# Kernel optimization log

Measured on AMD Instinct MI355X. Metric: run time of the kernel, lower is better.

Reference implementation:

```python
import jax, jax.numpy as jnp
import numpy as np

N_ATOMS = 50000
N_PAIRS = 1000000
F = 128        # n_atombasis
K = 64         # n_radialbasis
B = 5          # graph_n_blocks
NRI = 3        # residual layers (interaction)
NRF = 2        # residual layers (features)
_LOG2 = float(np.log(2.0))


def ssp(x):
    # shifted softplus: log(0.5*exp(x) + 0.5)
    return jax.nn.softplus(x) - _LOG2


def setup_inputs() -> dict:
    key = jax.random.key(0)
    ks = jax.random.split(key, 24)
    s = 0.1
    f32 = jnp.float32
    inp = {
        'features': jax.random.normal(ks[0], (N_ATOMS, F), f32),
        'cutoffs': jax.random.uniform(ks[1], (N_PAIRS,), f32),
        'rbfs': jax.random.uniform(ks[2], (N_PAIRS, K), f32),
        'idx_i': jnp.sort(jax.random.randint(ks[3], (N_PAIRS,), 0, N_ATOMS)),
        'idx_j': jax.random.randint(ks[4], (N_PAIRS,), 0, N_ATOMS),
        # per-block parameters (leading dim = block)
        'Wg': jax.random.normal(ks[5], (B, K, F), f32) * s,      # rbf filter, no bias
        'Wi': jax.random.normal(ks[6], (B, F, F), f32) * s,
        'bi': jnp.zeros((B, F), f32),
        'Wj': jax.random.normal(ks[7], (B, F, F), f32) * s,
        'bj': jnp.zeros((B, F), f32),
        'Wr1': jax.random.normal(ks[8], (B, NRI, F, F), f32) * s,
        'br1': jnp.zeros((B, NRI, F), f32),
        'Wr2': jax.random.normal(ks[9], (B, NRI, F, F), f32) * s,
        'br2': jnp.zeros((B, NRI, F), f32),
        'Wout': jax.random.normal(ks[10], (B, F, F), f32) * s,
        'bout': jnp.zeros((B, F), f32),
        'u': jnp.ones((B, F), f32),                               # gated skip
        'Wf1': jax.random.normal(ks[11], (B, NRF, F, F), f32) * s,
        'bf1': jnp.zeros((B, NRF, F), f32),
        'Wf2': jax.random.normal(ks[12], (B, NRF, F, F), f32) * s,
        'bf2': jnp.zeros((B, NRF, F), f32),
    }
    return inp


def _physnet_forward(features, cutoffs, rbfs, idx_i, idx_j,
                     Wg, Wi, bi, Wj, bj, Wr1, br1, Wr2, br2,
                     Wout, bout, u, Wf1, bf1, Wf2, bf2):
    descriptors = cutoffs[:, None] * rbfs           # [P, K]
    x = features
    outs = []
    for b in range(B):
        xa = ssp(x)
        g = descriptors @ Wg[b]                     # [P, F]
        xi = ssp(xa @ Wi[b] + bi[b])                # [N, F]
        xj = ssp(xa @ Wj[b] + bj[b])                # [N, F]
        msg = g * xj[idx_j]                         # gather-transform, [P, F]
        m = xi + jax.ops.segment_sum(msg, idx_i, num_segments=N_ATOMS)
        for r in range(NRI):                        # residual (interaction)
            m = m + ssp(ssp(m) @ Wr1[b, r] + br1[b, r]) @ Wr2[b, r] + br2[b, r]
        m = ssp(m)
        x = u[b] * x + m @ Wout[b] + bout[b]        # gated update
        for r in range(NRF):                        # residual (features)
            x = x + ssp(ssp(x) @ Wf1[b, r] + bf1[b, r]) @ Wf2[b, r] + bf2[b, r]
        outs.append(x)
    return jnp.stack(outs, axis=0)                  # [B, N, F] == features_list


def reference(features, cutoffs, rbfs, idx_i, idx_j,
              Wg, Wi, bi, Wj, bj, Wr1, br1, Wr2, br2,
              Wout, bout, u, Wf1, bf1, Wf2, bf2):
    return _physnet_forward(features, cutoffs, rbfs, idx_i, idx_j,
                            Wg, Wi, bi, Wj, bj, Wr1, br1, Wr2, br2,
                            Wout, bout, u, Wf1, bf1, Wf2, bf2)
```

## Files before the change

kernel.cpp:

```cpp
#include <hip/hip_runtime.h>
#include <math.h>

#define NA 50000
#define NP 1000000
#define FD 128
#define KD 64
#define NB 5
#define NRI_ 3
#define NRF_ 2

typedef short short8_t __attribute__((ext_vector_type(8)));
typedef short short4_t __attribute__((ext_vector_type(4)));
typedef float f32x4 __attribute__((ext_vector_type(4)));

__device__ __forceinline__ float sspf(float x) {
    float t = __logf(__expf(-fabsf(x)) + 1.0f);
    return fmaxf(x, 0.0f) + (t - 0.69314718055994530942f);
}

__device__ __forceinline__ unsigned cvt_pk_bf16(float lo, float hi) {
    unsigned r;
    asm("v_cvt_pk_bf16_f32 %0, %1, %2" : "=v"(r) : "v"(lo), "v"(hi));
    return r;
}

__device__ __forceinline__ short f2bf(float f) {
    unsigned r;
    asm("v_cvt_pk_bf16_f32 %0, %1, %1" : "=v"(r) : "v"(f));
    return (short)r;
}

__global__ void transpose_weights(const float* __restrict__ src,
                                  short* __restrict__ dst, int K)
{
    const size_t mo = (size_t)blockIdx.x * K * 128;
    const float* s = src + mo;
    short* d = dst + mo;
    for (int e = threadIdx.x; e < K * 128; e += 256) {
        int k = e >> 7, n = e & 127;
        d[n * K + k] = f2bf(s[e]);
    }
}

__global__ void prep_desc(const float* __restrict__ rbfs,
                          const float* __restrict__ cutoffs,
                          short* __restrict__ desc)
{
    long long c = (long long)blockIdx.x * 256 + threadIdx.x;
    if (c >= (long long)NP * 8) return;
    long long pair = c >> 3;
    float cu = cutoffs[pair];
    const float* s = rbfs + c * 8;
    float4 a = *(const float4*)s;
    float4 b = *(const float4*)(s + 4);
    int4 pk;
    pk.x = (int)cvt_pk_bf16(a.x * cu, a.y * cu);
    pk.y = (int)cvt_pk_bf16(a.z * cu, a.w * cu);
    pk.z = (int)cvt_pk_bf16(b.x * cu, b.y * cu);
    pk.w = (int)cvt_pk_bf16(b.z * cu, b.w * cu);
    *(int4*)&desc[c * 8] = pk;
}

__device__ __forceinline__ void stage_wt(const short* __restrict__ WT,
                                         short* wt_s, int tid)
{
#pragma unroll
    for (int i = 0; i < 8; ++i) {
        int c = i * 256 + tid;
        int n = c >> 4, kc = c & 15;
        *(short8_t*)&wt_s[n * 136 + kc * 8] = *(const short8_t*)&WT[n * 128 + kc * 8];
    }
}

__device__ __forceinline__ void gemm16(const short* actw, const short* wt_s,
                                       int mI, int quad, f32x4 acc[8])
{
#pragma unroll
    for (int ch = 0; ch < 4; ++ch) {
        short8_t a = *(const short8_t*)&actw[mI * 136 + ch * 32 + quad * 8];
#pragma unroll
        for (int ct = 0; ct < 8; ++ct) {
            short8_t bf = *(const short8_t*)&wt_s[(ct * 16 + mI) * 136 + ch * 32 + quad * 8];
            acc[ct] = __builtin_amdgcn_mfma_f32_16x16x32_bf16(a, bf, acc[ct], 0, 0, 0);
        }
    }
}

__launch_bounds__(256, 3)
__global__ void pre_kernel(const float* __restrict__ x,
                           const short* __restrict__ WiT, const float* __restrict__ bi_,
                           const short* __restrict__ WjT, const float* __restrict__ bj_,
                           float* __restrict__ xi_out, float* __restrict__ xj_out)
{
    __shared__ short act_s[64 * 136];
    __shared__ short wt_s[128 * 136];
    const int tid = threadIdx.x;
    const int lane = tid & 63, wv = tid >> 6;
    const int mI = lane & 15, quad = lane >> 4;
    const short* actw = act_s + wv * 16 * 136;
    const int row0 = blockIdx.x * 64;
    const int rowrd = row0 + wv * 16 + quad * 4;

#pragma unroll
    for (int i = 0; i < 8; ++i) {
        int f = i * 256 + tid;
        int rr = f >> 5;
        int c4 = (f & 31) * 4;
        float4 v = make_float4(0.f, 0.f, 0.f, 0.f);
        if (row0 + rr < NA) v = *(const float4*)&x[(size_t)(row0 + rr) * FD + c4];
        int2 pk;
        pk.x = (int)cvt_pk_bf16(sspf(v.x), sspf(v.y));
        pk.y = (int)cvt_pk_bf16(sspf(v.z), sspf(v.w));
        *(int2*)&act_s[rr * 136 + c4] = pk;
    }
    stage_wt(WiT, wt_s, tid);
    __syncthreads();

    f32x4 acc[8];
#pragma unroll
    for (int ct = 0; ct < 8; ++ct) acc[ct] = (f32x4){0.f, 0.f, 0.f, 0.f};
    gemm16(actw, wt_s, mI, quad, acc);
#pragma unroll
    for (int ct = 0; ct < 8; ++ct) {
        float bb = bi_[ct * 16 + mI];
#pragma unroll
        for (int rg = 0; rg < 4; ++rg) {
            int r = rowrd + rg;
            if (r < NA) xi_out[(size_t)r * FD + ct * 16 + mI] = sspf(acc[ct][rg] + bb);
        }
    }
    __syncthreads();
    stage_wt(WjT, wt_s, tid);
    __syncthreads();
#pragma unroll
    for (int ct = 0; ct < 8; ++ct) acc[ct] = (f32x4){0.f, 0.f, 0.f, 0.f};
    gemm16(actw, wt_s, mI, quad, acc);
#pragma unroll
    for (int ct = 0; ct < 8; ++ct) {
        float bb = bj_[ct * 16 + mI];
#pragma unroll
        for (int rg = 0; rg < 4; ++rg) {
            int r = rowrd + rg;
            if (r < NA) xj_out[(size_t)r * FD + ct * 16 + mI] = sspf(acc[ct][rg] + bb);
        }
    }
}

template<bool TAIL>
__launch_bounds__(256, 3)
__global__ void chain_kernel(const float* __restrict__ xprev,
                             const float* __restrict__ mbuf,
                             const short* __restrict__ Wr1T, const float* __restrict__ br1_,
                             const short* __restrict__ Wr2T, const float* __restrict__ br2_,
                             const short* __restrict__ WoT,  const float* __restrict__ bo_,
                             const float* __restrict__ u_,
                             const short* __restrict__ Wf1T, const float* __restrict__ bf1_,
                             const short* __restrict__ Wf2T, const float* __restrict__ bf2_,
                             float* __restrict__ xout,
                             const short* __restrict__ WiT, const float* __restrict__ bi_,
                             const short* __restrict__ WjT, const float* __restrict__ bj_,
                             float* __restrict__ xi_out, float* __restrict__ xj_out)
{
    __shared__ short act_s[64 * 136];
    __shared__ short wt_s[128 * 136];
    const int tid = threadIdx.x;
    const int lane = tid & 63, wv = tid >> 6;
    const int mI = lane & 15, quad = lane >> 4;
    short* actw = act_s + wv * 16 * 136;
    const int rowrd = blockIdx.x * 64 + wv * 16 + quad * 4;

    float mreg[8][4];
#pragma unroll
    for (int ct = 0; ct < 8; ++ct)
#pragma unroll
        for (int rg = 0; rg < 4; ++rg) {
            int r = rowrd + rg;
            mreg[ct][rg] = (r < NA) ? mbuf[(size_t)r * FD + ct * 16 + mI] : 0.f;
        }

    f32x4 acc[8];

    for (int r = 0; r < NRI_; ++r) {
        __syncthreads();
        stage_wt(Wr1T + (size_t)r * FD * FD, wt_s, tid);
#pragma unroll
        for (int ct = 0; ct < 8; ++ct)
#pragma unroll
            for (int rg = 0; rg < 4; ++rg)
                actw[(quad * 4 + rg) * 136 + ct * 16 + mI] = f2bf(sspf(mreg[ct][rg]));
        __syncthreads();
#pragma unroll
        for (int ct = 0; ct < 8; ++ct) acc[ct] = (f32x4){0.f, 0.f, 0.f, 0.f};
        gemm16(actw, wt_s, mI, quad, acc);

        __syncthreads();
        stage_wt(Wr2T + (size_t)r * FD * FD, wt_s, tid);
#pragma unroll
        for (int ct = 0; ct < 8; ++ct) {
            float b1 = br1_[r * FD + ct * 16 + mI];
#pragma unroll
            for (int rg = 0; rg < 4; ++rg)
                actw[(quad * 4 + rg) * 136 + ct * 16 + mI] = f2bf(sspf(acc[ct][rg] + b1));
        }
        __syncthreads();
#pragma unroll
        for (int ct = 0; ct < 8; ++ct) acc[ct] = (f32x4){0.f, 0.f, 0.f, 0.f};
        gemm16(actw, wt_s, mI, quad, acc);
#pragma unroll
        for (int ct = 0; ct < 8; ++ct) {
            float b2 = br2_[r * FD + ct * 16 + mI];
#pragma unroll
            for (int rg = 0; rg < 4; ++rg)
                mreg[ct][rg] += acc[ct][rg] + b2;
        }
    }

    __syncthreads();
    stage_wt(WoT, wt_s, tid);
#pragma unroll
    for (int ct = 0; ct < 8; ++ct)
#pragma unroll
        for (int rg = 0; rg < 4; ++rg)
            actw[(quad * 4 + rg) * 136 + ct * 16 + mI] = f2bf(sspf(mreg[ct][rg]));
    __syncthreads();
#pragma unroll
    for (int ct = 0; ct < 8; ++ct) acc[ct] = (f32x4){0.f, 0.f, 0.f, 0.f};
    gemm16(actw, wt_s, mI, quad, acc);

    float xreg[8][4];
#pragma unroll
    for (int ct = 0; ct < 8; ++ct) {
        float bo = bo_[ct * 16 + mI];
        float uu = u_[ct * 16 + mI];
#pragma unroll
        for (int rg = 0; rg < 4; ++rg) {
            int r = rowrd + rg;
            float xp = (r < NA) ? xprev[(size_t)r * FD + ct * 16 + mI] : 0.f;
            xreg[ct][rg] = fmaf(uu, xp, acc[ct][rg] + bo);
        }
    }

    for (int r = 0; r < NRF_; ++r) {
        __syncthreads();
        stage_wt(Wf1T + (size_t)r * FD * FD, wt_s, tid);
#pragma unroll
        for (int ct = 0; ct < 8; ++ct)
#pragma unroll
            for (int rg = 0; rg < 4; ++rg)
                actw[(quad * 4 + rg) * 136 + ct * 16 + mI] = f2bf(sspf(xreg[ct][rg]));
        __syncthreads();
#pragma unroll
        for (int ct = 0; ct < 8; ++ct) acc[ct] = (f32x4){0.f, 0.f, 0.f, 0.f};
        gemm16(actw, wt_s, mI, quad, acc);

        __syncthreads();
        stage_wt(Wf2T + (size_t)r * FD * FD, wt_s, tid);
#pragma unroll
        for (int ct = 0; ct < 8; ++ct) {
            float b1 = bf1_[r * FD + ct * 16 + mI];
#pragma unroll
            for (int rg = 0; rg < 4; ++rg)
                actw[(quad * 4 + rg) * 136 + ct * 16 + mI] = f2bf(sspf(acc[ct][rg] + b1));
        }
        __syncthreads();
#pragma unroll
        for (int ct = 0; ct < 8; ++ct) acc[ct] = (f32x4){0.f, 0.f, 0.f, 0.f};
        gemm16(actw, wt_s, mI, quad, acc);
#pragma unroll
        for (int ct = 0; ct < 8; ++ct) {
            float b2 = bf2_[r * FD + ct * 16 + mI];
#pragma unroll
            for (int rg = 0; rg < 4; ++rg)
                xreg[ct][rg] += acc[ct][rg] + b2;
        }
    }

#pragma unroll
    for (int ct = 0; ct < 8; ++ct)
#pragma unroll
        for (int rg = 0; rg < 4; ++rg) {
            int r = rowrd + rg;
            if (r < NA) xout[(size_t)r * FD + ct * 16 + mI] = xreg[ct][rg];
        }

    if constexpr (TAIL) {
        __syncthreads();
        stage_wt(WiT, wt_s, tid);
#pragma unroll
        for (int ct = 0; ct < 8; ++ct)
#pragma unroll
            for (int rg = 0; rg < 4; ++rg)
                actw[(quad * 4 + rg) * 136 + ct * 16 + mI] = f2bf(sspf(xreg[ct][rg]));
        __syncthreads();
#pragma unroll
        for (int ct = 0; ct < 8; ++ct) acc[ct] = (f32x4){0.f, 0.f, 0.f, 0.f};
        gemm16(actw, wt_s, mI, quad, acc);
#pragma unroll
        for (int ct = 0; ct < 8; ++ct) {
            float bb = bi_[ct * 16 + mI];
#pragma unroll
            for (int rg = 0; rg < 4; ++rg) {
                int r = rowrd + rg;
                if (r < NA) xi_out[(size_t)r * FD + ct * 16 + mI] = sspf(acc[ct][rg] + bb);
            }
        }
        __syncthreads();
        stage_wt(WjT, wt_s, tid);
        __syncthreads();
#pragma unroll
        for (int ct = 0; ct < 8; ++ct) acc[ct] = (f32x4){0.f, 0.f, 0.f, 0.f};
        gemm16(actw, wt_s, mI, quad, acc);
#pragma unroll
        for (int ct = 0; ct < 8; ++ct) {
            float bb = bj_[ct * 16 + mI];
#pragma unroll
            for (int rg = 0; rg < 4; ++rg) {
                int r = rowrd + rg;
                if (r < NA) xj_out[(size_t)r * FD + ct * 16 + mI] = sspf(acc[ct][rg] + bb);
            }
        }
    }
}

template<bool DESC>
__launch_bounds__(256, 4)
__global__ void pair_mfma(const float* __restrict__ rbfs,
                          const float* __restrict__ cutoffs,
                          const short* __restrict__ desc,
                          const int* __restrict__ idx_i,
                          const int* __restrict__ idx_j,
                          const short* __restrict__ WgT,
                          const float* __restrict__ xj,
                          float* __restrict__ mout)
{
    __shared__ float g_s[64 * 132];
    __shared__ int ii_s[128];
    __shared__ int jj_s[128];
    short* wt_s = (short*)g_s;

    const int tid = threadIdx.x;
    const long long p0 = (long long)blockIdx.x * 128;

#pragma unroll
    for (int i = 0; i < 4; ++i) {
        int c = i * 256 + tid;
        int n = c >> 3, kc = c & 7;
        *(short8_t*)&wt_s[n * 72 + kc * 8] = *(const short8_t*)&WgT[n * 64 + kc * 8];
    }
    if (tid < 128) {
        long long pg = p0 + tid;
        ii_s[tid] = (pg < NP) ? idx_i[pg] : -1;
        jj_s[tid] = (pg < NP) ? idx_j[pg] : 0;
    }
    __syncthreads();

    const int lane = tid & 63, wv = tid >> 6;
    const int m = lane & 15, quad = lane >> 4;

    f32x4 acc[2][8];
#pragma unroll
    for (int rt = 0; rt < 2; ++rt)
#pragma unroll
        for (int ct = 0; ct < 8; ++ct) acc[rt][ct] = (f32x4){0.f, 0.f, 0.f, 0.f};

#pragma unroll
    for (int chunk = 0; chunk < 2; ++chunk) {
        short8_t afr[2];
#pragma unroll
        for (int rt = 0; rt < 2; ++rt) {
            long long pg = p0 + wv * 32 + rt * 16 + m;
            if constexpr (DESC) {
                if (pg < NP) {
                    afr[rt] = *(const short8_t*)&desc[pg * KD + chunk * 32 + quad * 8];
                } else {
                    int4 z = make_int4(0, 0, 0, 0);
                    afr[rt] = __builtin_bit_cast(short8_t, z);
                }
            } else {
                float v[8];
                if (pg < NP) {
                    const float* ap = rbfs + pg * KD + chunk * 32 + quad * 8;
                    float4 x0 = *(const float4*)ap;
                    float4 x1 = *(const float4*)(ap + 4);
                    float cu = cutoffs[pg];
                    v[0] = x0.x * cu; v[1] = x0.y * cu; v[2] = x0.z * cu; v[3] = x0.w * cu;
                    v[4] = x1.x * cu; v[5] = x1.y * cu; v[6] = x1.z * cu; v[7] = x1.w * cu;
                } else {
#pragma unroll
                    for (int j = 0; j < 8; ++j) v[j] = 0.f;
                }
                int4 pk = make_int4((int)cvt_pk_bf16(v[0], v[1]),
                                    (int)cvt_pk_bf16(v[2], v[3]),
                                    (int)cvt_pk_bf16(v[4], v[5]),
                                    (int)cvt_pk_bf16(v[6], v[7]));
                afr[rt] = __builtin_bit_cast(short8_t, pk);
            }
        }
#pragma unroll
        for (int ct = 0; ct < 8; ++ct) {
            short8_t bfr = *(short8_t*)&wt_s[(ct * 16 + m) * 72 + chunk * 32 + quad * 8];
            acc[0][ct] = __builtin_amdgcn_mfma_f32_16x16x32_bf16(afr[0], bfr, acc[0][ct], 0, 0, 0);
            acc[1][ct] = __builtin_amdgcn_mfma_f32_16x16x32_bf16(afr[1], bfr, acc[1][ct], 0, 0, 0);
        }
    }
    __syncthreads();

    const int tx = tid & 15, ty = tid >> 4;
    const int c0 = tx * 4, c1 = c0 + 64;
    const int col = tid & 127, sh = tid >> 7;

#pragma unroll
    for (int h = 0; h < 2; ++h) {
        if ((wv >> 1) == h) {
#pragma unroll
            for (int ct = 0; ct < 8; ++ct) {
                int cg = ct * 16 + m;
#pragma unroll
                for (int rt = 0; rt < 2; ++rt) {
                    int lp = (wv & 1) * 32 + rt * 16 + quad * 4;
#pragma unroll
                    for (int rg = 0; rg < 4; ++rg)
                        g_s[(lp + rg) * 132 + cg] = acc[rt][ct][rg];
                }
            }
        }
        __syncthreads();
#pragma unroll
        for (int i = 0; i < 4; ++i) {
            int p = ty + 16 * i;
            int jrow = jj_s[h * 64 + p];
            float4 xa = *(const float4*)&xj[(size_t)jrow * FD + c0];
            float4 xb = *(const float4*)&xj[(size_t)jrow * FD + c1];
            float4 ga = *(float4*)&g_s[p * 132 + c0];
            float4 gb = *(float4*)&g_s[p * 132 + c1];
            ga.x *= xa.x; ga.y *= xa.y; ga.z *= xa.z; ga.w *= xa.w;
            gb.x *= xb.x; gb.y *= xb.y; gb.z *= xb.z; gb.w *= xb.w;
            *(float4*)&g_s[p * 132 + c0] = ga;
            *(float4*)&g_s[p * 132 + c1] = gb;
        }
        __syncthreads();
        {
            int base = h * 64 + sh * 32;
            float accum = 0.f;
            int cur = ii_s[base];
            for (int q = 0; q < 32; ++q) {
                int a = ii_s[base + q];
                if (a != cur) {
                    if (cur >= 0) atomicAdd(&mout[(size_t)cur * FD + col], accum);
                    accum = 0.f;
                    cur = a;
                }
                accum += g_s[(sh * 32 + q) * 132 + col];
            }
            if (cur >= 0) atomicAdd(&mout[(size_t)cur * FD + col], accum);
        }
        if (h == 0) __syncthreads();
    }
}

extern "C" void kernel_launch(void* const* d_in, const int* in_sizes, int n_in,
                              void* d_out, int out_size, void* d_ws, size_t ws_size,
                              hipStream_t stream)
{
    const float* features = (const float*)d_in[0];
    const float* cutoffs  = (const float*)d_in[1];
    const float* rbfs     = (const float*)d_in[2];
    const int*   idx_i    = (const int*)d_in[3];
    const int*   idx_j    = (const int*)d_in[4];
    const float* Wg   = (const float*)d_in[5];
    const float* Wi   = (const float*)d_in[6];
    const float* bi   = (const float*)d_in[7];
    const float* Wj   = (const float*)d_in[8];
    const float* bj   = (const float*)d_in[9];
    const float* Wr1  = (const float*)d_in[10];
    const float* br1  = (const float*)d_in[11];
    const float* Wr2  = (const float*)d_in[12];
    const float* br2  = (const float*)d_in[13];
    const float* Wout = (const float*)d_in[14];
    const float* bout = (const float*)d_in[15];
    const float* u    = (const float*)d_in[16];
    const float* Wf1  = (const float*)d_in[17];
    const float* bf1  = (const float*)d_in[18];
    const float* Wf2  = (const float*)d_in[19];
    const float* bf2  = (const float*)d_in[20];
    float* out = (float*)d_out;

    const size_t NF = (size_t)NA * FD;
    const size_t MS = (size_t)FD * FD;
    float* mbuf = (float*)d_ws;
    short* wtb  = (short*)(mbuf + NF);
    short* wgt  = wtb + 65 * MS;
    short* desc = wgt + (size_t)NB * FD * KD;
    float* xjbuf = out + 4 * NF;

    const size_t base_bytes = NF * 4 + 65 * MS * 2 + (size_t)NB * FD * KD * 2;
    const size_t desc_bytes = (size_t)NP * KD * 2;
    const bool use_desc = ws_size >= base_bytes + desc_bytes;

    transpose_weights<<<5,  256, 0, stream>>>(Wi,   wtb +  0 * MS, 128);
    transpose_weights<<<5,  256, 0, stream>>>(Wj,   wtb +  5 * MS, 128);
    transpose_weights<<<15, 256, 0, stream>>>(Wr1,  wtb + 10 * MS, 128);
    transpose_weights<<<15, 256, 0, stream>>>(Wr2,  wtb + 25 * MS, 128);
    transpose_weights<<<5,  256, 0, stream>>>(Wout, wtb + 40 * MS, 128);
    transpose_weights<<<10, 256, 0, stream>>>(Wf1,  wtb + 45 * MS, 128);
    transpose_weights<<<10, 256, 0, stream>>>(Wf2,  wtb + 55 * MS, 128);
    transpose_weights<<<5,  256, 0, stream>>>(Wg,   wgt, 64);
    if (use_desc) {
        prep_desc<<<(int)(((long long)NP * 8 + 255) / 256), 256, 0, stream>>>(rbfs, cutoffs, desc);
    }

    const int gA = (NA + 63) / 64;
    const int gP = (NP + 127) / 128;
    dim3 blk(256);

    pre_kernel<<<gA, blk, 0, stream>>>(features,
        wtb + 0 * MS, bi, wtb + 5 * MS, bj, mbuf, xjbuf);

    const float* x = features;
    for (int b = 0; b < NB; ++b) {
        float* xout = out + (size_t)b * NF;

        if (use_desc) {
            pair_mfma<true><<<gP, blk, 0, stream>>>(rbfs, cutoffs, desc, idx_i, idx_j,
                wgt + (size_t)b * FD * KD, xjbuf, mbuf);
        } else {
            pair_mfma<false><<<gP, blk, 0, stream>>>(rbfs, cutoffs, desc, idx_i, idx_j,
                wgt + (size_t)b * FD * KD, xjbuf, mbuf);
        }

        if (b < NB - 1) {
            chain_kernel<true><<<gA, blk, 0, stream>>>(x, mbuf,
                wtb + (10 + b * NRI_) * MS, br1 + (size_t)b * NRI_ * FD,
                wtb + (25 + b * NRI_) * MS, br2 + (size_t)b * NRI_ * FD,
                wtb + (40 + b) * MS, bout + (size_t)b * FD, u + (size_t)b * FD,
                wtb + (45 + b * NRF_) * MS, bf1 + (size_t)b * NRF_ * FD,
                wtb + (55 + b * NRF_) * MS, bf2 + (size_t)b * NRF_ * FD,
                xout,
                wtb + (0 + (b + 1)) * MS, bi + (size_t)(b + 1) * FD,
                wtb + (5 + (b + 1)) * MS, bj + (size_t)(b + 1) * FD,
                mbuf, xjbuf);
        } else {
            chain_kernel<false><<<gA, blk, 0, stream>>>(x, mbuf,
                wtb + (10 + b * NRI_) * MS, br1 + (size_t)b * NRI_ * FD,
                wtb + (25 + b * NRI_) * MS, br2 + (size_t)b * NRI_ * FD,
                wtb + (40 + b) * MS, bout + (size_t)b * FD, u + (size_t)b * FD,
                wtb + (45 + b * NRF_) * MS, bf1 + (size_t)b * NRF_ * FD,
                wtb + (55 + b * NRF_) * MS, bf2 + (size_t)b * NRF_ * FD,
                xout,
                (const short*)nullptr, (const float*)nullptr,
                (const short*)nullptr, (const float*)nullptr,
                (float*)nullptr, (float*)nullptr);
        }
        x = xout;
    }
}
```

Before: 2.113 ms.

## Pre-swizzle weights and descriptors into MFMA fragment order, read from global

Weights and the rbf descriptor buffer are now pre-packed into the exact per-lane MFMA B/A fragment order, so each lane loads one contiguous 16-byte vector straight from global or L2. The kernels drop LDS weight staging along with most of their __syncthreads, and occupancy hints rise from 3 to 4 blocks because LDS use shrinks. The trade-off is that weight fragments are re-read from cache by every wave instead of being shared through LDS, which adds L2 traffic and load latency to the MFMA loops. Removing the barriers also depends on each wave touching only its own slice of act_s.

```diff
diff --git a/kernel.cpp b/kernel.cpp
--- a/kernel.cpp
+++ b/kernel.cpp
@@ -10,7 +10,6 @@
 #define NRF_ 2
 
 typedef short short8_t __attribute__((ext_vector_type(8)));
-typedef short short4_t __attribute__((ext_vector_type(4)));
 typedef float f32x4 __attribute__((ext_vector_type(4)));
 
 __device__ __forceinline__ float sspf(float x) {
@@ -30,27 +29,40 @@
     return (short)r;
 }
 
-__global__ void transpose_weights(const float* __restrict__ src,
-                                  short* __restrict__ dst, int K)
-{
-    const size_t mo = (size_t)blockIdx.x * K * 128;
-    const float* s = src + mo;
-    short* d = dst + mo;
-    for (int e = threadIdx.x; e < K * 128; e += 256) {
-        int k = e >> 7, n = e & 127;
-        d[n * K + k] = f2bf(s[e]);
+__global__ void frag_weights(const float* __restrict__ src,
+                             short* __restrict__ dst, int kch)
+{
+    const int nchunk = kch * 512;
+    const float* s = src + (size_t)blockIdx.x * kch * 4096;
+    short* d = dst + (size_t)blockIdx.x * kch * 4096;
+    for (int c = threadIdx.x; c < nchunk; c += 256) {
+        int lane = c & 63, ct = (c >> 6) & 7, ch = c >> 9;
+        int quad = lane >> 4, mI = lane & 15;
+        const float* sp = s + (ch * 32 + quad * 8) * 128 + ct * 16 + mI;
+        float v[8];
+#pragma unroll
+        for (int j = 0; j < 8; ++j) v[j] = sp[j * 128];
+        int4 pk = make_int4((int)cvt_pk_bf16(v[0], v[1]),
+                            (int)cvt_pk_bf16(v[2], v[3]),
+                            (int)cvt_pk_bf16(v[4], v[5]),
+                            (int)cvt_pk_bf16(v[6], v[7]));
+        *(short8_t*)&d[c * 8] = __builtin_bit_cast(short8_t, pk);
     }
 }
 
 __global__ void prep_desc(const float* __restrict__ rbfs,
                           const float* __restrict__ cutoffs,
-                          short* __restrict__ desc)
+                          short* __restrict__ descF)
 {
     long long c = (long long)blockIdx.x * 256 + threadIdx.x;
     if (c >= (long long)NP * 8) return;
-    long long pair = c >> 3;
-    float cu = cutoffs[pair];
-    const float* s = rbfs + c * 8;
+    int lane = (int)(c & 63);
+    int chunk = (int)((c >> 6) & 1);
+    long long t16 = c >> 7;
+    int quad = lane >> 4, mI = lane & 15;
+    long long p = t16 * 16 + mI;
+    float cu = cutoffs[p];
+    const float* s = rbfs + p * KD + chunk * 32 + quad * 8;
     float4 a = *(const float4*)s;
     float4 b = *(const float4*)(s + 4);
     int4 pk;
@@ -58,42 +70,32 @@
     pk.y = (int)cvt_pk_bf16(a.z * cu, a.w * cu);
     pk.z = (int)cvt_pk_bf16(b.x * cu, b.y * cu);
     pk.w = (int)cvt_pk_bf16(b.z * cu, b.w * cu);
-    *(int4*)&desc[c * 8] = pk;
-}
-
-__device__ __forceinline__ void stage_wt(const short* __restrict__ WT,
-                                         short* wt_s, int tid)
-{
-#pragma unroll
-    for (int i = 0; i < 8; ++i) {
-        int c = i * 256 + tid;
-        int n = c >> 4, kc = c & 15;
-        *(short8_t*)&wt_s[n * 136 + kc * 8] = *(const short8_t*)&WT[n * 128 + kc * 8];
-    }
-}
-
-__device__ __forceinline__ void gemm16(const short* actw, const short* wt_s,
-                                       int mI, int quad, f32x4 acc[8])
+    *(short8_t*)&descF[c * 8] = __builtin_bit_cast(short8_t, pk);
+}
+
+__device__ __forceinline__ void gemm16_direct(const short* actw,
+                                              const short* __restrict__ WF,
+                                              int mI, int quad, int lane,
+                                              f32x4 acc[8])
 {
 #pragma unroll
     for (int ch = 0; ch < 4; ++ch) {
         short8_t a = *(const short8_t*)&actw[mI * 136 + ch * 32 + quad * 8];
 #pragma unroll
         for (int ct = 0; ct < 8; ++ct) {
-            short8_t bf = *(const short8_t*)&wt_s[(ct * 16 + mI) * 136 + ch * 32 + quad * 8];
+            short8_t bf = *(const short8_t*)&WF[((ch * 8 + ct) * 64 + lane) * 8];
             acc[ct] = __builtin_amdgcn_mfma_f32_16x16x32_bf16(a, bf, acc[ct], 0, 0, 0);
         }
     }
 }
 
-__launch_bounds__(256, 3)
+__launch_bounds__(256, 4)
 __global__ void pre_kernel(const float* __restrict__ x,
-                           const short* __restrict__ WiT, const float* __restrict__ bi_,
-                           const short* __restrict__ WjT, const float* __restrict__ bj_,
+                           const short* __restrict__ WiF, const float* __restrict__ bi_,
+                           const short* __restrict__ WjF, const float* __restrict__ bj_,
                            float* __restrict__ xi_out, float* __restrict__ xj_out)
 {
     __shared__ short act_s[64 * 136];
-    __shared__ short wt_s[128 * 136];
     const int tid = threadIdx.x;
     const int lane = tid & 63, wv = tid >> 6;
     const int mI = lane & 15, quad = lane >> 4;
@@ -113,13 +115,12 @@
         pk.y = (int)cvt_pk_bf16(sspf(v.z), sspf(v.w));
         *(int2*)&act_s[rr * 136 + c4] = pk;
     }
-    stage_wt(WiT, wt_s, tid);
     __syncthreads();
 
     f32x4 acc[8];
 #pragma unroll
     for (int ct = 0; ct < 8; ++ct) acc[ct] = (f32x4){0.f, 0.f, 0.f, 0.f};
-    gemm16(actw, wt_s, mI, quad, acc);
+    gemm16_direct(actw, WiF, mI, quad, lane, acc);
 #pragma unroll
     for (int ct = 0; ct < 8; ++ct) {
         float bb = bi_[ct * 16 + mI];
@@ -129,12 +130,9 @@
             if (r < NA) xi_out[(size_t)r * FD + ct * 16 + mI] = sspf(acc[ct][rg] + bb);
         }
     }
-    __syncthreads();
-    stage_wt(WjT, wt_s, tid);
-    __syncthreads();
 #pragma unroll
     for (int ct = 0; ct < 8; ++ct) acc[ct] = (f32x4){0.f, 0.f, 0.f, 0.f};
-    gemm16(actw, wt_s, mI, quad, acc);
+    gemm16_direct(actw, WjF, mI, quad, lane, acc);
 #pragma unroll
     for (int ct = 0; ct < 8; ++ct) {
         float bb = bj_[ct * 16 + mI];
@@ -147,22 +145,21 @@
 }
 
 template<bool TAIL>
-__launch_bounds__(256, 3)
+__launch_bounds__(256, 4)
 __global__ void chain_kernel(const float* __restrict__ xprev,
                              const float* __restrict__ mbuf,
-                             const short* __restrict__ Wr1T, const float* __restrict__ br1_,
-                             const short* __restrict__ Wr2T, const float* __restrict__ br2_,
-                             const short* __restrict__ WoT,  const float* __restrict__ bo_,
+                             const short* __restrict__ Wr1F, const float* __restrict__ br1_,
+                             const short* __restrict__ Wr2F, const float* __restrict__ br2_,
+                             const short* __restrict__ WoF,  const float* __restrict__ bo_,
                              const float* __restrict__ u_,
-                             const short* __restrict__ Wf1T, const float* __restrict__ bf1_,
-                             const short* __restrict__ Wf2T, const float* __restrict__ bf2_,
+                             const short* __restrict__ Wf1F, const float* __restrict__ bf1_,
+                             const short* __restrict__ Wf2F, const float* __restrict__ bf2_,
                              float* __restrict__ xout,
-                             const short* __restrict__ WiT, const float* __restrict__ bi_,
-                             const short* __restrict__ WjT, const float* __restrict__ bj_,
+                             const short* __restrict__ WiF, const float* __restrict__ bi_,
+                             const short* __restrict__ WjF, const float* __restrict__ bj_,
                              float* __restrict__ xi_out, float* __restrict__ xj_out)
 {
     __shared__ short act_s[64 * 136];
-    __shared__ short wt_s[128 * 136];
     const int tid = threadIdx.x;
     const int lane = tid & 63, wv = tid >> 6;
     const int mI = lane & 15, quad = lane >> 4;
@@ -181,20 +178,15 @@
     f32x4 acc[8];
 
     for (int r = 0; r < NRI_; ++r) {
-        __syncthreads();
-        stage_wt(Wr1T + (size_t)r * FD * FD, wt_s, tid);
 #pragma unroll
         for (int ct = 0; ct < 8; ++ct)
 #pragma unroll
             for (int rg = 0; rg < 4; ++rg)
                 actw[(quad * 4 + rg) * 136 + ct * 16 + mI] = f2bf(sspf(mreg[ct][rg]));
-        __syncthreads();
 #pragma unroll
         for (int ct = 0; ct < 8; ++ct) acc[ct] = (f32x4){0.f, 0.f, 0.f, 0.f};
-        gemm16(actw, wt_s, mI, quad, acc);
-
-        __syncthreads();
-        stage_wt(Wr2T + (size_t)r * FD * FD, wt_s, tid);
+        gemm16_direct(actw, Wr1F + (size_t)r * FD * FD, mI, quad, lane, acc);
+
 #pragma unroll
         for (int ct = 0; ct < 8; ++ct) {
             float b1 = br1_[r * FD + ct * 16 + mI];
@@ -202,10 +194,9 @@
             for (int rg = 0; rg < 4; ++rg)
                 actw[(quad * 4 + rg) * 136 + ct * 16 + mI] = f2bf(sspf(acc[ct][rg] + b1));
         }
-        __syncthreads();
 #pragma unroll
         for (int ct = 0; ct < 8; ++ct) acc[ct] = (f32x4){0.f, 0.f, 0.f, 0.f};
-        gemm16(actw, wt_s, mI, quad, acc);
+        gemm16_direct(actw, Wr2F + (size_t)r * FD * FD, mI, quad, lane, acc);
 #pragma unroll
         for (int ct = 0; ct < 8; ++ct) {
             float b2 = br2_[r * FD + ct * 16 + mI];
@@ -215,17 +206,14 @@
         }
     }
 
-    __syncthreads();
-    stage_wt(WoT, wt_s, tid);
 #pragma unroll
     for (int ct = 0; ct < 8; ++ct)
 #pragma unroll
         for (int rg = 0; rg < 4; ++rg)
             actw[(quad * 4 + rg) * 136 + ct * 16 + mI] = f2bf(sspf(mreg[ct][rg]));
-    __syncthreads();
 #pragma unroll
     for (int ct = 0; ct < 8; ++ct) acc[ct] = (f32x4){0.f, 0.f, 0.f, 0.f};
-    gemm16(actw, wt_s, mI, quad, acc);
+    gemm16_direct(actw, WoF, mI, quad, lane, acc);
 
     float xreg[8][4];
 #pragma unroll
@@ -241,20 +229,15 @@
     }
 
     for (int r = 0; r < NRF_; ++r) {
-        __syncthreads();
-        stage_wt(Wf1T + (size_t)r * FD * FD, wt_s, tid);
 #pragma unroll
         for (int ct = 0; ct < 8; ++ct)
 #pragma unroll
             for (int rg = 0; rg < 4; ++rg)
                 actw[(quad * 4 + rg) * 136 + ct * 16 + mI] = f2bf(sspf(xreg[ct][rg]));
-        __syncthreads();
 #pragma unroll
         for (int ct = 0; ct < 8; ++ct) acc[ct] = (f32x4){0.f, 0.f, 0.f, 0.f};
-        gemm16(actw, wt_s, mI, quad, acc);
-
-        __syncthreads();
-        stage_wt(Wf2T + (size_t)r * FD * FD, wt_s, tid);
+        gemm16_direct(actw, Wf1F + (size_t)r * FD * FD, mI, quad, lane, acc);
+
 #pragma unroll
         for (int ct = 0; ct < 8; ++ct) {
             float b1 = bf1_[r * FD + ct * 16 + mI];
@@ -262,10 +245,9 @@
             for (int rg = 0; rg < 4; ++rg)
                 actw[(quad * 4 + rg) * 136 + ct * 16 + mI] = f2bf(sspf(acc[ct][rg] + b1));
         }
-        __syncthreads();
 #pragma unroll
         for (int ct = 0; ct < 8; ++ct) acc[ct] = (f32x4){0.f, 0.f, 0.f, 0.f};
-        gemm16(actw, wt_s, mI, quad, acc);
+        gemm16_direct(actw, Wf2F + (size_t)r * FD * FD, mI, quad, lane, acc);
 #pragma unroll
         for (int ct = 0; ct < 8; ++ct) {
             float b2 = bf2_[r * FD + ct * 16 + mI];
@@ -284,17 +266,14 @@
         }
 
     if constexpr (TAIL) {
-        __syncthreads();
-        stage_wt(WiT, wt_s, tid);
 #pragma unroll
         for (int ct = 0; ct < 8; ++ct)
 #pragma unroll
             for (int rg = 0; rg < 4; ++rg)
                 actw[(quad * 4 + rg) * 136 + ct * 16 + mI] = f2bf(sspf(xreg[ct][rg]));
-        __syncthreads();
 #pragma unroll
         for (int ct = 0; ct < 8; ++ct) acc[ct] = (f32x4){0.f, 0.f, 0.f, 0.f};
-        gemm16(actw, wt_s, mI, quad, acc);
+        gemm16_direct(actw, WiF, mI, quad, lane, acc);
 #pragma unroll
         for (int ct = 0; ct < 8; ++ct) {
             float bb = bi_[ct * 16 + mI];
@@ -304,12 +283,9 @@
                 if (r < NA) xi_out[(size_t)r * FD + ct * 16 + mI] = sspf(acc[ct][rg] + bb);
             }
         }
-        __syncthreads();
-        stage_wt(WjT, wt_s, tid);
-        __syncthreads();
 #pragma unroll
         for (int ct = 0; ct < 8; ++ct) acc[ct] = (f32x4){0.f, 0.f, 0.f, 0.f};
-        gemm16(actw, wt_s, mI, quad, acc);
+        gemm16_direct(actw, WjF, mI, quad, lane, acc);
 #pragma unroll
         for (int ct = 0; ct < 8; ++ct) {
             float bb = bj_[ct * 16 + mI];
@@ -326,33 +302,25 @@
 __launch_bounds__(256, 4)
 __global__ void pair_mfma(const float* __restrict__ rbfs,
                           const float* __restrict__ cutoffs,
-                          const short* __restrict__ desc,
+                          const short* __restrict__ descF,
                           const int* __restrict__ idx_i,
                           const int* __restrict__ idx_j,
-                          const short* __restrict__ WgT,
+                          const short* __restrict__ WgF,
                           const float* __restrict__ xj,
                           float* __restrict__ mout)
 {
     __shared__ float g_s[64 * 132];
     __shared__ int ii_s[128];
     __shared__ int jj_s[128];
-    short* wt_s = (short*)g_s;
 
     const int tid = threadIdx.x;
     const long long p0 = (long long)blockIdx.x * 128;
 
-#pragma unroll
-    for (int i = 0; i < 4; ++i) {
-        int c = i * 256 + tid;
-        int n = c >> 3, kc = c & 7;
-        *(short8_t*)&wt_s[n * 72 + kc * 8] = *(const short8_t*)&WgT[n * 64 + kc * 8];
-    }
     if (tid < 128) {
         long long pg = p0 + tid;
         ii_s[tid] = (pg < NP) ? idx_i[pg] : -1;
         jj_s[tid] = (pg < NP) ? idx_j[pg] : 0;
     }
-    __syncthreads();
 
     const int lane = tid & 63, wv = tid >> 6;
     const int m = lane & 15, quad = lane >> 4;
@@ -368,15 +336,16 @@
         short8_t afr[2];
 #pragma unroll
         for (int rt = 0; rt < 2; ++rt) {
-            long long pg = p0 + wv * 32 + rt * 16 + m;
             if constexpr (DESC) {
-                if (pg < NP) {
-                    afr[rt] = *(const short8_t*)&desc[pg * KD + chunk * 32 + quad * 8];
+                long long tg = (long long)blockIdx.x * 8 + wv * 2 + rt;
+                if (tg < (long long)NP / 16) {
+                    afr[rt] = *(const short8_t*)&descF[((tg * 2 + chunk) * 64 + lane) * 8];
                 } else {
                     int4 z = make_int4(0, 0, 0, 0);
                     afr[rt] = __builtin_bit_cast(short8_t, z);
                 }
             } else {
+                long long pg = p0 + wv * 32 + rt * 16 + m;
                 float v[8];
                 if (pg < NP) {
                     const float* ap = rbfs + pg * KD + chunk * 32 + quad * 8;
@@ -398,12 +367,11 @@
         }
 #pragma unroll
         for (int ct = 0; ct < 8; ++ct) {
-            short8_t bfr = *(short8_t*)&wt_s[(ct * 16 + m) * 72 + chunk * 32 + quad * 8];
+            short8_t bfr = *(const short8_t*)&WgF[((chunk * 8 + ct) * 64 + lane) * 8];
             acc[0][ct] = __builtin_amdgcn_mfma_f32_16x16x32_bf16(afr[0], bfr, acc[0][ct], 0, 0, 0);
             acc[1][ct] = __builtin_amdgcn_mfma_f32_16x16x32_bf16(afr[1], bfr, acc[1][ct], 0, 0, 0);
         }
     }
-    __syncthreads();
 
     const int tx = tid & 15, ty = tid >> 4;
     const int c0 = tx * 4, c1 = c0 + 64;
@@ -497,14 +465,14 @@
     const size_t desc_bytes = (size_t)NP * KD * 2;
     const bool use_desc = ws_size >= base_bytes + desc_bytes;
 
-    transpose_weights<<<5,  256, 0, stream>>>(Wi,   wtb +  0 * MS, 128);
-    transpose_weights<<<5,  256, 0, stream>>>(Wj,   wtb +  5 * MS, 128);
-    transpose_weights<<<15, 256, 0, stream>>>(Wr1,  wtb + 10 * MS, 128);
-    transpose_weights<<<15, 256, 0, stream>>>(Wr2,  wtb + 25 * MS, 128);
-    transpose_weights<<<5,  256, 0, stream>>>(Wout, wtb + 40 * MS, 128);
-    transpose_weights<<<10, 256, 0, stream>>>(Wf1,  wtb + 45 * MS, 128);
-    transpose_weights<<<10, 256, 0, stream>>>(Wf2,  wtb + 55 * MS, 128);
-    transpose_weights<<<5,  256, 0, stream>>>(Wg,   wgt, 64);
+    frag_weights<<<5,  256, 0, stream>>>(Wi,   wtb +  0 * MS, 4);
+    frag_weights<<<5,  256, 0, stream>>>(Wj,   wtb +  5 * MS, 4);
+    frag_weights<<<15, 256, 0, stream>>>(Wr1,  wtb + 10 * MS, 4);
+    frag_weights<<<15, 256, 0, stream>>>(Wr2,  wtb + 25 * MS, 4);
+    frag_weights<<<5,  256, 0, stream>>>(Wout, wtb + 40 * MS, 4);
+    frag_weights<<<10, 256, 0, stream>>>(Wf1,  wtb + 45 * MS, 4);
+    frag_weights<<<10, 256, 0, stream>>>(Wf2,  wtb + 55 * MS, 4);
+    frag_weights<<<5,  256, 0, stream>>>(Wg,   wgt, 2);
     if (use_desc) {
         prep_desc<<<(int)(((long long)NP * 8 + 255) / 256), 256, 0, stream>>>(rbfs, cutoffs, desc);
     }
```

Measured after the change: 1.806 ms. 1.17x faster.
